# Kernel optimization log

Hardware: AMD Instinct MI355X
Metric: run time of the kernel (lower is better)

## Reference

```python
import jax, jax.numpy as jnp
import numpy as np

N_IN, N_OUT, H, EMB, NSC = 32, 8, 256, 32, 5
B, T = 256, 512
D_IN0 = N_IN + N_OUT + EMB  # 72


def setup_inputs() -> dict:
    key = jax.random.key(0)
    ks = jax.random.split(key, 18)
    s = 0.05
    rn = lambda k, shape: (jax.random.normal(k, shape, jnp.float32) * s)
    return {
        "x_cv": jax.random.normal(ks[0], (B, T, N_IN), jnp.float32),
        "pv_init": jax.random.normal(ks[1], (B, N_OUT), jnp.float32),
        "scenario": jax.random.randint(ks[2], (B,), 0, NSC),
        "emb_table": rn(ks[3], (NSC, EMB)),
        "W_ih0": rn(ks[4], (4 * H, D_IN0)),
        "W_hh0": rn(ks[5], (4 * H, H)),
        "b_ih0": rn(ks[6], (4 * H,)),
        "b_hh0": rn(ks[7], (4 * H,)),
        "W_ih1": rn(ks[8], (4 * H, H)),
        "W_hh1": rn(ks[9], (4 * H, H)),
        "b_ih1": rn(ks[10], (4 * H,)),
        "b_hh1": rn(ks[11], (4 * H,)),
        "fc1_w": rn(ks[12], (H // 2, H)),
        "fc1_b": rn(ks[13], (H // 2,)),
        "fc2_w": rn(ks[14], (N_OUT, H // 2)),
        "fc2_b": rn(ks[15], (N_OUT,)),
    }


def _lstm_cell(x, h, c, W_ih, W_hh, b):
    # torch gate order: i, f, g, o
    g = x @ W_ih.T + h @ W_hh.T + b
    i, f, gg, o = jnp.split(g, 4, axis=-1)
    c_new = jax.nn.sigmoid(f) * c + jax.nn.sigmoid(i) * jnp.tanh(gg)
    h_new = jax.nn.sigmoid(o) * jnp.tanh(c_new)
    return h_new, c_new


def reference(x_cv, pv_init, scenario, emb_table, W_ih0, W_hh0, b_ih0, b_hh0,
              W_ih1, W_hh1, b_ih1, b_hh1, fc1_w, fc1_b, fc2_w, fc2_b):
    # previous prediction. Dropout inactive (eval mode).
    emb = emb_table[scenario]          # [B, EMB]
    b0 = b_ih0 + b_hh0
    b1 = b_ih1 + b_hh1
    Bsz = x_cv.shape[0]
    z = jnp.zeros((Bsz, H), x_cv.dtype)

    def step(carry, x_t):
        h0, c0, h1, c1, pv = carry
        xt = jnp.concatenate([x_t, pv, emb], axis=-1)   # [B, D_IN0]
        h0, c0 = _lstm_cell(xt, h0, c0, W_ih0, W_hh0, b0)
        h1, c1 = _lstm_cell(h0, h1, c1, W_ih1, W_hh1, b1)
        pv_pred = jax.nn.relu(h1 @ fc1_w.T + fc1_b) @ fc2_w.T + fc2_b
        new_carry = (h0, c0, h1, c1, jax.lax.stop_gradient(pv_pred))
        return new_carry, pv_pred

    init = (z, z, z, z, pv_init)
    _, outs = jax.lax.scan(step, init, jnp.swapaxes(x_cv, 0, 1))  # [T, B, N_OUT]
    return jnp.swapaxes(outs, 0, 1)  # [B, T, N_OUT]
```

## Files before the change

### kernel.cpp

```cpp
#include <hip/hip_runtime.h>
#include <hip/hip_bf16.h>


#define B_TOT   256
#define T_STEPS 512
#define NIN     32
#define NOUT    8
#define HDIM    256
#define EMBD    32

#define BPG   2
#define NBLK  (B_TOT / BPG)
#define NTHR  256

#define K2_0      160
#define K2_0_REAL 148
#define NCH0      10
#define K2_1      256
#define NCH1      16

#define WT0_OFF   0u
#define WT0_BYTES (K2_0 * HDIM * 4u * 4u)
#define WT1_OFF   (WT0_OFF + WT0_BYTES)
#define WT1_BYTES (K2_1 * HDIM * 4u * 4u)
#define FC1_OFF   (WT1_OFF + WT1_BYTES)
#define FC1_BYTES (128u * 128u * 4u)
#define FC2_OFF   (FC1_OFF + FC1_BYTES)
#define FC2_BYTES (64u * 8u * 4u)

typedef _Float16 h2 __attribute__((ext_vector_type(2)));

#if __has_builtin(__builtin_amdgcn_fdot2)
#define FDOT2(a, b, c) __builtin_amdgcn_fdot2((a), (b), (c), false)
#else
#define FDOT2(a, b, c) ((c) + (float)(a).x * (float)(b).x + (float)(a).y * (float)(b).y)
#endif

__device__ __forceinline__ float sigm(float x) {
    return 1.0f / (1.0f + __expf(-x));
}
__device__ __forceinline__ float tanh_fast(float x) {
    float e = __expf(2.0f * x);
    return 1.0f - 2.0f / (e + 1.0f);
}

__global__ void prep_wt0(const float* __restrict__ Wih0,
                         const float* __restrict__ Whh0,
                         h2* __restrict__ wt0) {
    int hidx = blockIdx.x * blockDim.x + threadIdx.x;
    if (hidx >= K2_0 * 1024) return;
    int g = hidx & 3, uu = (hidx >> 2) & 255, k2 = hidx >> 10;
    h2 r = {(_Float16)0.0f, (_Float16)0.0f};
    if (k2 < K2_0_REAL) {
        int row = g * 256 + uu;
        int k = 2 * k2;
        float v0 = (k < 40)     ? Wih0[row * 72 + k]     : Whh0[row * 256 + (k - 40)];
        float v1 = (k + 1 < 40) ? Wih0[row * 72 + k + 1] : Whh0[row * 256 + (k + 1 - 40)];
        r.x = (_Float16)v0;
        r.y = (_Float16)v1;
    }
    wt0[hidx] = r;
}

__global__ void prep_wt1(const float* __restrict__ Wih1,
                         const float* __restrict__ Whh1,
                         h2* __restrict__ wt1) {
    int hidx = blockIdx.x * blockDim.x + threadIdx.x;
    if (hidx >= K2_1 * 1024) return;
    int g = hidx & 3, uu = (hidx >> 2) & 255, k2 = hidx >> 10;
    int row = g * 256 + uu;
    int k = 2 * k2;
    float v0 = (k < 256)     ? Wih1[row * 256 + k]           : Whh1[row * 256 + (k - 256)];
    float v1 = (k + 1 < 256) ? Wih1[row * 256 + k + 1]       : Whh1[row * 256 + (k + 1 - 256)];
    h2 r;
    r.x = (_Float16)v0;
    r.y = (_Float16)v1;
    wt1[hidx] = r;
}

__global__ void prep_fc(const float* __restrict__ fc1w,
                        const float* __restrict__ fc2w,
                        h2* __restrict__ f1t,
                        h2* __restrict__ f2t) {
    int hidx = blockIdx.x * blockDim.x + threadIdx.x;
    if (hidx < 16384) {
        int r = hidx & 127, k2 = hidx >> 7;
        h2 v;
        v.x = (_Float16)fc1w[r * 256 + 2 * k2];
        v.y = (_Float16)fc1w[r * 256 + 2 * k2 + 1];
        f1t[hidx] = v;
    } else if (hidx < 16384 + 512) {
        int hi = hidx - 16384;
        int j = hi & 7, k2 = hi >> 3;
        h2 v;
        v.x = (_Float16)fc2w[j * 128 + 2 * k2];
        v.y = (_Float16)fc2w[j * 128 + 2 * k2 + 1];
        f2t[hi] = v;
    }
}

__device__ __forceinline__ void load16(float4 (&buf)[16],
                                       const float4* __restrict__ wt,
                                       int k2b, int u) {
#pragma unroll
    for (int j = 0; j < 16; ++j) buf[j] = wt[(k2b + j) * 256 + u];
}

template <int S>
__device__ __forceinline__ void comp16(const float4 (&buf)[16],
                                       const h2* xt, int k2b,
                                       float (&acc)[4][BPG]) {
#pragma unroll
    for (int j = 0; j < 16; ++j) {
        h2 w0 = __builtin_bit_cast(h2, buf[j].x);
        h2 w1 = __builtin_bit_cast(h2, buf[j].y);
        h2 w2 = __builtin_bit_cast(h2, buf[j].z);
        h2 w3 = __builtin_bit_cast(h2, buf[j].w);
#pragma unroll
        for (int i = 0; i < BPG; ++i) {
            h2 xv = xt[i * S + k2b + j];
            acc[0][i] = FDOT2(w0, xv, acc[0][i]);
            acc[1][i] = FDOT2(w1, xv, acc[1][i]);
            acc[2][i] = FDOT2(w2, xv, acc[2][i]);
            acc[3][i] = FDOT2(w3, xv, acc[3][i]);
        }
    }
}

template <int S>
__device__ __forceinline__ void matvec_pipe(const float4* __restrict__ wt,
                                            const h2* xt, int NCH, int u,
                                            float (&acc)[4][BPG]) {
    float4 A[16], Bb[16];
    load16(A, wt, 0, u);
    int c = 0;
    for (; c + 2 < NCH; c += 2) {
        load16(Bb, wt, (c + 1) * 16, u);
        comp16<S>(A, xt, c * 16, acc);
        load16(A, wt, (c + 2) * 16, u);
        comp16<S>(Bb, xt, (c + 1) * 16, acc);
    }
    if (NCH & 1) {
        comp16<S>(A, xt, (NCH - 1) * 16, acc);
    } else {
        load16(Bb, wt, (NCH - 1) * 16, u);
        comp16<S>(A, xt, (NCH - 2) * 16, acc);
        comp16<S>(Bb, xt, (NCH - 1) * 16, acc);
    }
}

__global__ __launch_bounds__(NTHR, 1) void lstm_main(
    const float* __restrict__ x_cv, const float* __restrict__ pv_init,
    const int* __restrict__ scen, const float* __restrict__ emb_table,
    const float* __restrict__ Wih0, const float* __restrict__ b_ih0,
    const float* __restrict__ b_hh0, const float* __restrict__ b_ih1,
    const float* __restrict__ b_hh1, const float* __restrict__ fc1_b,
    const float* __restrict__ fc2_b, const float4* __restrict__ wt0,
    const float4* __restrict__ wt1, const h2* __restrict__ fc1t,
    const h2* __restrict__ fc2t, float* __restrict__ out) {
    __shared__ h2 xt0[BPG][K2_0];
    __shared__ h2 xt1[BPG][K2_1];
    __shared__ h2 fch[BPG][64];
    __shared__ float h0f[BPG][HDIM];
    __shared__ float h1f[BPG][HDIM];
    __shared__ float fc1o[BPG][128];
    __shared__ float pvf[BPG][NOUT];
    __shared__ float embs[BPG][EMBD];

    const int tid = threadIdx.x;
    const int u = tid;
    const int b0 = blockIdx.x * BPG;

    {
        h2 z = {(_Float16)0.0f, (_Float16)0.0f};
        {
            int i = tid >> 7, p = tid & 127;
            xt0[i][20 + p] = z;
        }
        for (int idx = tid; idx < BPG * K2_1; idx += NTHR) {
            int i = idx >> 8, p = idx & 255;
            xt1[i][p] = z;
        }
        if (tid < BPG * 12) {
            int i = tid / 12, p = tid % 12;
            xt0[i][K2_0_REAL + p] = z;
        }
        if (tid < BPG * NOUT) {
            int i = tid >> 3, j = tid & 7;
            pvf[i][j] = pv_init[(b0 + i) * NOUT + j];
        }
        if (tid < BPG * EMBD) {
            int i = tid >> 5, kk = tid & 31;
            embs[i][kk] = emb_table[scen[b0 + i] * EMBD + kk];
        }
    }
    __syncthreads();

    float bias0[4][BPG], bias1g[4];
#pragma unroll
    for (int g = 0; g < 4; ++g) {
        const int row = g * 256 + u;
        bias1g[g] = b_ih1[row] + b_hh1[row];
        float s0 = b_ih0[row] + b_hh0[row];
        float s1 = s0;
        for (int kk = 0; kk < EMBD; ++kk) {
            float w = Wih0[row * 72 + 40 + kk];
            s0 += embs[0][kk] * w;
            s1 += embs[1][kk] * w;
        }
        bias0[g][0] = s0;
        bias0[g][1] = s1;
    }

    const float fc1bias = fc1_b[tid & 127];
    float fc2bias = 0.0f;
    float* outp = nullptr;
    if (tid < BPG * NOUT) {
        int j = tid & 7, i = tid >> 3;
        fc2bias = fc2_b[j];
        outp = out + ((size_t)(b0 + i) * T_STEPS) * NOUT + j;
    }

    float c0v[BPG] = {0.0f, 0.0f};
    float c1v[BPG] = {0.0f, 0.0f};

    for (int t = 0; t < T_STEPS; ++t) {
        if (tid < BPG * 20) {
            int i = tid / 20, k2l = tid % 20;
            h2 v;
            if (k2l < 16) {
                const float* xp =
                    x_cv + ((size_t)(b0 + i) * T_STEPS + t) * NIN + 2 * k2l;
                v.x = (_Float16)xp[0];
                v.y = (_Float16)xp[1];
            } else {
                v.x = (_Float16)pvf[i][2 * (k2l - 16)];
                v.y = (_Float16)pvf[i][2 * (k2l - 16) + 1];
            }
            xt0[i][k2l] = v;
        }
        __syncthreads();

        float acc[4][BPG];
#pragma unroll
        for (int g = 0; g < 4; ++g)
#pragma unroll
            for (int i = 0; i < BPG; ++i) acc[g][i] = bias0[g][i];
        matvec_pipe<K2_0>(wt0, &xt0[0][0], NCH0, u, acc);

#pragma unroll
        for (int i = 0; i < BPG; ++i) {
            float ig = sigm(acc[0][i]);
            float fg = sigm(acc[1][i]);
            float gg = tanh_fast(acc[2][i]);
            float og = sigm(acc[3][i]);
            float cn = fg * c0v[i] + ig * gg;
            c0v[i] = cn;
            h0f[i][u] = og * tanh_fast(cn);
        }
        __syncthreads();

        {
            int i = tid >> 7, p = tid & 127;
            h2 v;
            v.x = (_Float16)h0f[i][2 * p];
            v.y = (_Float16)h0f[i][2 * p + 1];
            xt0[i][20 + p] = v;
            xt1[i][p] = v;
        }
        __syncthreads();

#pragma unroll
        for (int g = 0; g < 4; ++g)
#pragma unroll
            for (int i = 0; i < BPG; ++i) acc[g][i] = bias1g[g];
        matvec_pipe<K2_1>(wt1, &xt1[0][0], NCH1, u, acc);

#pragma unroll
        for (int i = 0; i < BPG; ++i) {
            float ig = sigm(acc[0][i]);
            float fg = sigm(acc[1][i]);
            float gg = tanh_fast(acc[2][i]);
            float og = sigm(acc[3][i]);
            float cn = fg * c1v[i] + ig * gg;
            c1v[i] = cn;
            h1f[i][u] = og * tanh_fast(cn);
        }
        __syncthreads();

        {
            int i = tid >> 7, p = tid & 127;
            h2 v;
            v.x = (_Float16)h1f[i][2 * p];
            v.y = (_Float16)h1f[i][2 * p + 1];
            xt1[i][128 + p] = v;
        }
        __syncthreads();

        {
            int r = tid & 127, i = tid >> 7;
            float a = fc1bias;
            const h2* xrow = &xt1[i][128];
#pragma unroll 8
            for (int k2 = 0; k2 < 128; ++k2)
                a = FDOT2(fc1t[k2 * 128 + r], xrow[k2], a);
            fc1o[i][r] = fmaxf(a, 0.0f);
        }
        __syncthreads();

        if (tid < BPG * 64) {
            int i = tid >> 6, p = tid & 63;
            h2 v;
            v.x = (_Float16)fc1o[i][2 * p];
            v.y = (_Float16)fc1o[i][2 * p + 1];
            fch[i][p] = v;
        }
        __syncthreads();

        if (tid < BPG * NOUT) {
            int j = tid & 7, i = tid >> 3;
            float a = fc2bias;
#pragma unroll 8
            for (int k2 = 0; k2 < 64; ++k2)
                a = FDOT2(fc2t[k2 * 8 + j], fch[i][k2], a);
            outp[(size_t)t * NOUT] = a;
            pvf[i][j] = a;
        }
        __syncthreads();
    }
}

extern "C" void kernel_launch(void* const* d_in, const int* in_sizes, int n_in,
                              void* d_out, int out_size, void* d_ws,
                              size_t ws_size, hipStream_t stream) {
    const float* x_cv = (const float*)d_in[0];
    const float* pv_init = (const float*)d_in[1];
    const int* scen = (const int*)d_in[2];
    const float* embt = (const float*)d_in[3];
    const float* Wih0 = (const float*)d_in[4];
    const float* Whh0 = (const float*)d_in[5];
    const float* bih0 = (const float*)d_in[6];
    const float* bhh0 = (const float*)d_in[7];
    const float* Wih1 = (const float*)d_in[8];
    const float* Whh1 = (const float*)d_in[9];
    const float* bih1 = (const float*)d_in[10];
    const float* bhh1 = (const float*)d_in[11];
    const float* fc1w = (const float*)d_in[12];
    const float* fc1b = (const float*)d_in[13];
    const float* fc2w = (const float*)d_in[14];
    const float* fc2b = (const float*)d_in[15];

    char* ws = (char*)d_ws;
    h2* wt0 = (h2*)(ws + WT0_OFF);
    h2* wt1 = (h2*)(ws + WT1_OFF);
    h2* f1t = (h2*)(ws + FC1_OFF);
    h2* f2t = (h2*)(ws + FC2_OFF);

    prep_wt0<<<(K2_0 * 1024) / 256, 256, 0, stream>>>(Wih0, Whh0, wt0);
    prep_wt1<<<(K2_1 * 1024) / 256, 256, 0, stream>>>(Wih1, Whh1, wt1);
    prep_fc<<<66, 256, 0, stream>>>(fc1w, fc2w, f1t, f2t);

    lstm_main<<<NBLK, NTHR, 0, stream>>>(
        x_cv, pv_init, scen, embt, Wih0, bih0, bhh0, bih1, bhh1, fc1b, fc2b,
        (const float4*)wt0, (const float4*)wt1, f1t, f2t, (float*)d_out);
}
```

Baseline: 15.63 ms.

## Split LSTM hidden units across blocks with LDS-resident weights and global flag sync

The kernel is rebuilt so that each group of 16 batch rows is handled by 16 cooperating blocks. Each block owns a 16-unit slice of the hidden state for every gate and keeps its fp16 weight slice resident in LDS, instead of streaming all weights from global memory every step. Blocks exchange h0, h1 and the predicted pv through workspace buffers using acquire/release flag spin-waits each timestep. This trades weight bandwidth for inter-block synchronization latency. It also depends on all 256 blocks being co-resident, or the spin-waits will deadlock.

```diff
diff --git a/kernel.cpp b/kernel.cpp
--- a/kernel.cpp
+++ b/kernel.cpp
@@ -2,337 +2,373 @@
 #include <hip/hip_bf16.h>
 
 
-#define B_TOT   256
-#define T_STEPS 512
-#define NIN     32
-#define NOUT    8
-#define HDIM    256
-#define EMBD    32
-
-#define BPG   2
-#define NBLK  (B_TOT / BPG)
-#define NTHR  256
-
-#define K2_0      160
-#define K2_0_REAL 148
-#define NCH0      10
-#define K2_1      256
-#define NCH1      16
-
-#define WT0_OFF   0u
-#define WT0_BYTES (K2_0 * HDIM * 4u * 4u)
-#define WT1_OFF   (WT0_OFF + WT0_BYTES)
-#define WT1_BYTES (K2_1 * HDIM * 4u * 4u)
-#define FC1_OFF   (WT1_OFF + WT1_BYTES)
-#define FC1_BYTES (128u * 128u * 4u)
-#define FC2_OFF   (FC1_OFF + FC1_BYTES)
-#define FC2_BYTES (64u * 8u * 4u)
+#define TSTEPS 512
+#define NIN    32
 
 typedef _Float16 h2 __attribute__((ext_vector_type(2)));
-
 #if __has_builtin(__builtin_amdgcn_fdot2)
 #define FDOT2(a, b, c) __builtin_amdgcn_fdot2((a), (b), (c), false)
 #else
 #define FDOT2(a, b, c) ((c) + (float)(a).x * (float)(b).x + (float)(a).y * (float)(b).y)
 #endif
 
-__device__ __forceinline__ float sigm(float x) {
-    return 1.0f / (1.0f + __expf(-x));
-}
-__device__ __forceinline__ float tanh_fast(float x) {
+__device__ __forceinline__ float sigm(float x) { return 1.0f / (1.0f + __expf(-x)); }
+__device__ __forceinline__ float tanhf_(float x) {
     float e = __expf(2.0f * x);
     return 1.0f - 2.0f / (e + 1.0f);
 }
 
-__global__ void prep_wt0(const float* __restrict__ Wih0,
-                         const float* __restrict__ Whh0,
-                         h2* __restrict__ wt0) {
-    int hidx = blockIdx.x * blockDim.x + threadIdx.x;
-    if (hidx >= K2_0 * 1024) return;
-    int g = hidx & 3, uu = (hidx >> 2) & 255, k2 = hidx >> 10;
-    h2 r = {(_Float16)0.0f, (_Float16)0.0f};
-    if (k2 < K2_0_REAL) {
-        int row = g * 256 + uu;
-        int k = 2 * k2;
-        float v0 = (k < 40)     ? Wih0[row * 72 + k]     : Whh0[row * 256 + (k - 40)];
-        float v1 = (k + 1 < 40) ? Wih0[row * 72 + k + 1] : Whh0[row * 256 + (k + 1 - 40)];
-        r.x = (_Float16)v0;
-        r.y = (_Float16)v1;
-    }
-    wt0[hidx] = r;
-}
-
-__global__ void prep_wt1(const float* __restrict__ Wih1,
-                         const float* __restrict__ Whh1,
-                         h2* __restrict__ wt1) {
-    int hidx = blockIdx.x * blockDim.x + threadIdx.x;
-    if (hidx >= K2_1 * 1024) return;
-    int g = hidx & 3, uu = (hidx >> 2) & 255, k2 = hidx >> 10;
-    int row = g * 256 + uu;
-    int k = 2 * k2;
-    float v0 = (k < 256)     ? Wih1[row * 256 + k]           : Whh1[row * 256 + (k - 256)];
-    float v1 = (k + 1 < 256) ? Wih1[row * 256 + k + 1]       : Whh1[row * 256 + (k + 1 - 256)];
-    h2 r;
-    r.x = (_Float16)v0;
-    r.y = (_Float16)v1;
-    wt1[hidx] = r;
-}
-
-__global__ void prep_fc(const float* __restrict__ fc1w,
-                        const float* __restrict__ fc2w,
-                        h2* __restrict__ f1t,
-                        h2* __restrict__ f2t) {
-    int hidx = blockIdx.x * blockDim.x + threadIdx.x;
-    if (hidx < 16384) {
-        int r = hidx & 127, k2 = hidx >> 7;
-        h2 v;
-        v.x = (_Float16)fc1w[r * 256 + 2 * k2];
-        v.y = (_Float16)fc1w[r * 256 + 2 * k2 + 1];
-        f1t[hidx] = v;
-    } else if (hidx < 16384 + 512) {
-        int hi = hidx - 16384;
-        int j = hi & 7, k2 = hi >> 3;
-        h2 v;
-        v.x = (_Float16)fc2w[j * 128 + 2 * k2];
-        v.y = (_Float16)fc2w[j * 128 + 2 * k2 + 1];
-        f2t[hi] = v;
-    }
-}
-
-__device__ __forceinline__ void load16(float4 (&buf)[16],
-                                       const float4* __restrict__ wt,
-                                       int k2b, int u) {
-#pragma unroll
-    for (int j = 0; j < 16; ++j) buf[j] = wt[(k2b + j) * 256 + u];
-}
-
-template <int S>
-__device__ __forceinline__ void comp16(const float4 (&buf)[16],
-                                       const h2* xt, int k2b,
-                                       float (&acc)[4][BPG]) {
-#pragma unroll
-    for (int j = 0; j < 16; ++j) {
-        h2 w0 = __builtin_bit_cast(h2, buf[j].x);
-        h2 w1 = __builtin_bit_cast(h2, buf[j].y);
-        h2 w2 = __builtin_bit_cast(h2, buf[j].z);
-        h2 w3 = __builtin_bit_cast(h2, buf[j].w);
-#pragma unroll
-        for (int i = 0; i < BPG; ++i) {
-            h2 xv = xt[i * S + k2b + j];
-            acc[0][i] = FDOT2(w0, xv, acc[0][i]);
-            acc[1][i] = FDOT2(w1, xv, acc[1][i]);
-            acc[2][i] = FDOT2(w2, xv, acc[2][i]);
-            acc[3][i] = FDOT2(w3, xv, acc[3][i]);
-        }
-    }
-}
-
-template <int S>
-__device__ __forceinline__ void matvec_pipe(const float4* __restrict__ wt,
-                                            const h2* xt, int NCH, int u,
-                                            float (&acc)[4][BPG]) {
-    float4 A[16], Bb[16];
-    load16(A, wt, 0, u);
-    int c = 0;
-    for (; c + 2 < NCH; c += 2) {
-        load16(Bb, wt, (c + 1) * 16, u);
-        comp16<S>(A, xt, c * 16, acc);
-        load16(A, wt, (c + 2) * 16, u);
-        comp16<S>(Bb, xt, (c + 1) * 16, acc);
-    }
-    if (NCH & 1) {
-        comp16<S>(A, xt, (NCH - 1) * 16, acc);
+#define W0T_OFF 0u
+#define W1T_OFF 606208u
+#define F1T_OFF 1654784u
+#define F2T_OFF 1720320u
+#define HX0_OFF 2097152u
+#define HX1_OFF 2359296u
+#define PVX_OFF 2621440u
+#define FLG_OFF 2629632u
+#define WS_NEED 2678784u
+
+#define W0S 592
+#define W1S 1040
+#define X0S 608
+#define X1S 1040
+
+__global__ void prep_w(const float* __restrict__ Wih0, const float* __restrict__ Whh0,
+                       const float* __restrict__ Wih1, const float* __restrict__ Whh1,
+                       char* __restrict__ ws) {
+    int gid = blockIdx.x * 256 + threadIdx.x;
+    _Float16* w0 = (_Float16*)(ws + W0T_OFF);
+    _Float16* w1 = (_Float16*)(ws + W1T_OFF);
+    if (gid < 16 * 64 * 296) {
+        int k = gid % 296;
+        int rest = gid / 296;
+        int rl = rest & 63, j = rest >> 6;
+        int row = (rl >> 4) * 256 + j * 16 + (rl & 15);
+        float v;
+        if (k < 32) v = Wih0[row * 72 + k];
+        else if (k < 288) v = Whh0[row * 256 + (k - 32)];
+        else v = Wih0[row * 72 + 32 + (k - 288)];
+        w0[(j * 64 + rl) * 296 + k] = (_Float16)v;
     } else {
-        load16(Bb, wt, (NCH - 1) * 16, u);
-        comp16<S>(A, xt, (NCH - 2) * 16, acc);
-        comp16<S>(Bb, xt, (NCH - 1) * 16, acc);
-    }
-}
-
-__global__ __launch_bounds__(NTHR, 1) void lstm_main(
+        int gid2 = gid - 16 * 64 * 296;
+        if (gid2 < 16 * 64 * 512) {
+            int k = gid2 & 511;
+            int rest = gid2 >> 9;
+            int rl = rest & 63, j = rest >> 6;
+            int row = (rl >> 4) * 256 + j * 16 + (rl & 15);
+            float v = (k < 256) ? Wih1[row * 256 + k] : Whh1[row * 256 + (k - 256)];
+            w1[(j * 64 + rl) * 512 + k] = (_Float16)v;
+        }
+    }
+}
+
+__global__ void prep_fc(const float* __restrict__ fc1w, const float* __restrict__ fc2w,
+                        char* __restrict__ ws) {
+    int gid = blockIdx.x * 256 + threadIdx.x;
+    _Float16* f1 = (_Float16*)(ws + F1T_OFF);
+    _Float16* f2 = (_Float16*)(ws + F2T_OFF);
+    if (gid < 32768) {
+        int e = gid & 63, ks = (gid >> 6) & 3, r = gid >> 8;
+        f1[gid] = (_Float16)fc1w[r * 256 + ks * 64 + e];
+    } else if (gid < 32768 + 1024) {
+        int i = gid - 32768;
+        f2[i] = (_Float16)fc2w[i];
+    }
+}
+
+__global__ __launch_bounds__(512) void lstm_main(
     const float* __restrict__ x_cv, const float* __restrict__ pv_init,
     const int* __restrict__ scen, const float* __restrict__ emb_table,
     const float* __restrict__ Wih0, const float* __restrict__ b_ih0,
     const float* __restrict__ b_hh0, const float* __restrict__ b_ih1,
     const float* __restrict__ b_hh1, const float* __restrict__ fc1_b,
-    const float* __restrict__ fc2_b, const float4* __restrict__ wt0,
-    const float4* __restrict__ wt1, const h2* __restrict__ fc1t,
-    const h2* __restrict__ fc2t, float* __restrict__ out) {
-    __shared__ h2 xt0[BPG][K2_0];
-    __shared__ h2 xt1[BPG][K2_1];
-    __shared__ h2 fch[BPG][64];
-    __shared__ float h0f[BPG][HDIM];
-    __shared__ float h1f[BPG][HDIM];
-    __shared__ float fc1o[BPG][128];
-    __shared__ float pvf[BPG][NOUT];
-    __shared__ float embs[BPG][EMBD];
+    const float* __restrict__ fc2_b, char* __restrict__ ws,
+    float* __restrict__ out) {
+    struct __align__(16) SM {
+        char w0[64 * W0S];
+        char w1[64 * W1S];
+        char xt0[16 * X0S];
+        char xt1[16 * X1S];
+        float gates[16][64];
+        float biasE[16][64];
+        float bias1[64];
+        _Float16 htmp[16][16];
+        float embs[16][32];
+        float fc1o[128];
+        int scen_l[16];
+    };
+    __shared__ SM sm;
 
     const int tid = threadIdx.x;
-    const int u = tid;
-    const int b0 = blockIdx.x * BPG;
+    const int lane = tid & 63;
+    const int wv = tid >> 6;
+    const int bid = blockIdx.x;
+    const int g = (bid & 7) * 2 + ((bid >> 3) & 1);
+    const int j = bid >> 4;
+    const int B0 = g * 16;
+
+    const char* w0g = ws + W0T_OFF + (unsigned)j * (64u * 296u * 2u);
+    const char* w1g = ws + W1T_OFF + (unsigned)j * (64u * 512u * 2u);
+    unsigned long long* hx0 = (unsigned long long*)(ws + HX0_OFF) + (unsigned)g * 2u * 16u * 64u;
+    unsigned long long* hx1 = (unsigned long long*)(ws + HX1_OFF) + (unsigned)g * 2u * 16u * 64u;
+    unsigned long long* pvx = (unsigned long long*)(ws + PVX_OFF) + (unsigned)g * 2u * 16u * 2u;
+    unsigned int* flg = (unsigned int*)(ws + FLG_OFF) + (unsigned)g * 16u * 3u * 16u;
+
+    if (tid < 16) sm.scen_l[tid] = scen[B0 + tid];
+    if (tid == 0) {
+        __hip_atomic_store(&flg[(j * 3 + 0) * 16], 0u, __ATOMIC_RELAXED, __HIP_MEMORY_SCOPE_AGENT);
+        __hip_atomic_store(&flg[(j * 3 + 1) * 16], 0u, __ATOMIC_RELAXED, __HIP_MEMORY_SCOPE_AGENT);
+        __hip_atomic_store(&flg[(j * 3 + 2) * 16], 0u, __ATOMIC_RELAXED, __HIP_MEMORY_SCOPE_AGENT);
+    }
+    __syncthreads();
 
     {
-        h2 z = {(_Float16)0.0f, (_Float16)0.0f};
+        int b = tid >> 5, e = tid & 31;
+        sm.embs[b][e] = emb_table[sm.scen_l[b] * 32 + e];
+    }
+    for (int idx = tid; idx < (16 * X0S) / 8; idx += 512) ((unsigned long long*)sm.xt0)[idx] = 0ull;
+    for (int idx = tid; idx < (16 * X1S) / 8; idx += 512) ((unsigned long long*)sm.xt1)[idx] = 0ull;
+    for (int idx = tid; idx < 64 * 37; idx += 512) {
+        int r = idx / 37, c = idx - r * 37;
+        *(float4*)(&sm.w0[r * W0S + c * 16]) = *(const float4*)(w0g + r * 592 + c * 16);
+    }
+    for (int idx = tid; idx < 64 * 64; idx += 512) {
+        int r = idx >> 6, c = idx & 63;
+        *(float4*)(&sm.w1[r * W1S + c * 16]) = *(const float4*)(w1g + r * 1024 + c * 16);
+    }
+    __syncthreads();
+
+    for (int idx = tid; idx < 1024; idx += 512) {
+        int b = idx >> 6, rl = idx & 63;
+        int row = (rl >> 4) * 256 + j * 16 + (rl & 15);
+        float s = b_ih0[row] + b_hh0[row];
+        for (int e = 0; e < 32; ++e) s += sm.embs[b][e] * Wih0[row * 72 + 40 + e];
+        sm.biasE[b][rl] = s;
+    }
+    if (tid < 64) {
+        int row = (tid >> 4) * 256 + j * 16 + (tid & 15);
+        sm.bias1[tid] = b_ih1[row] + b_hh1[row];
+    }
+    float4 f1w[8];
+    {
+        const char* f1g = ws + F1T_OFF + (unsigned)tid * 128u;
+#pragma unroll
+        for (int q = 0; q < 8; ++q) f1w[q] = *(const float4*)(f1g + q * 16);
+    }
+    float f2w[16];
+    if (wv == 0) {
+        int jo = lane >> 3, ks2 = lane & 7;
+        const _Float16* f2g = (const _Float16*)(ws + F2T_OFF) + jo * 128 + ks2 * 16;
+#pragma unroll
+        for (int q = 0; q < 16; ++q) f2w[q] = (float)f2g[q];
+    }
+    const float fc2b_r = (wv == 0) ? fc2_b[lane >> 3] : 0.0f;
+    const float fc1b_r = fc1_b[tid >> 2];
+    float c0 = 0.0f, c1 = 0.0f;
+    __syncthreads();
+
+    for (int t = 0; t < TSTEPS; ++t) {
+        const int par = t & 1;
+
         {
-            int i = tid >> 7, p = tid & 127;
-            xt0[i][20 + p] = z;
-        }
-        for (int idx = tid; idx < BPG * K2_1; idx += NTHR) {
-            int i = idx >> 8, p = idx & 255;
-            xt1[i][p] = z;
-        }
-        if (tid < BPG * 12) {
-            int i = tid / 12, p = tid % 12;
-            xt0[i][K2_0_REAL + p] = z;
-        }
-        if (tid < BPG * NOUT) {
-            int i = tid >> 3, j = tid & 7;
-            pvf[i][j] = pv_init[(b0 + i) * NOUT + j];
-        }
-        if (tid < BPG * EMBD) {
-            int i = tid >> 5, kk = tid & 31;
-            embs[i][kk] = emb_table[scen[b0 + i] * EMBD + kk];
-        }
-    }
-    __syncthreads();
-
-    float bias0[4][BPG], bias1g[4];
-#pragma unroll
-    for (int g = 0; g < 4; ++g) {
-        const int row = g * 256 + u;
-        bias1g[g] = b_ih1[row] + b_hh1[row];
-        float s0 = b_ih0[row] + b_hh0[row];
-        float s1 = s0;
-        for (int kk = 0; kk < EMBD; ++kk) {
-            float w = Wih0[row * 72 + 40 + kk];
-            s0 += embs[0][kk] * w;
-            s1 += embs[1][kk] * w;
-        }
-        bias0[g][0] = s0;
-        bias0[g][1] = s1;
-    }
-
-    const float fc1bias = fc1_b[tid & 127];
-    float fc2bias = 0.0f;
-    float* outp = nullptr;
-    if (tid < BPG * NOUT) {
-        int j = tid & 7, i = tid >> 3;
-        fc2bias = fc2_b[j];
-        outp = out + ((size_t)(b0 + i) * T_STEPS) * NOUT + j;
-    }
-
-    float c0v[BPG] = {0.0f, 0.0f};
-    float c1v[BPG] = {0.0f, 0.0f};
-
-    for (int t = 0; t < T_STEPS; ++t) {
-        if (tid < BPG * 20) {
-            int i = tid / 20, k2l = tid % 20;
-            h2 v;
-            if (k2l < 16) {
-                const float* xp =
-                    x_cv + ((size_t)(b0 + i) * T_STEPS + t) * NIN + 2 * k2l;
-                v.x = (_Float16)xp[0];
-                v.y = (_Float16)xp[1];
+            int b = tid >> 5, k = tid & 31;
+            float xv = x_cv[((B0 + b) * TSTEPS + t) * NIN + k];
+            *(_Float16*)(&sm.xt0[b * X0S + k * 2]) = (_Float16)xv;
+        }
+        for (int idx = tid; idx < 1024; idx += 512) {
+            int b = idx >> 6, rl = idx & 63;
+            sm.gates[b][rl] = sm.biasE[b][rl];
+        }
+        if (wv == 0 && lane < 16) {
+            if (t == 0) {
+                const float* pp = pv_init + (B0 + lane) * 8;
+#pragma unroll
+                for (int q = 0; q < 8; ++q)
+                    *(_Float16*)(&sm.xt0[lane * X0S + (288 + q) * 2]) = (_Float16)pp[q];
             } else {
-                v.x = (_Float16)pvf[i][2 * (k2l - 16)];
-                v.y = (_Float16)pvf[i][2 * (k2l - 16) + 1];
-            }
-            xt0[i][k2l] = v;
-        }
-        __syncthreads();
-
-        float acc[4][BPG];
-#pragma unroll
-        for (int g = 0; g < 4; ++g)
-#pragma unroll
-            for (int i = 0; i < BPG; ++i) acc[g][i] = bias0[g][i];
-        matvec_pipe<K2_0>(wt0, &xt0[0][0], NCH0, u, acc);
-
-#pragma unroll
-        for (int i = 0; i < BPG; ++i) {
-            float ig = sigm(acc[0][i]);
-            float fg = sigm(acc[1][i]);
-            float gg = tanh_fast(acc[2][i]);
-            float og = sigm(acc[3][i]);
-            float cn = fg * c0v[i] + ig * gg;
-            c0v[i] = cn;
-            h0f[i][u] = og * tanh_fast(cn);
+                while (__hip_atomic_load(&flg[(lane * 3 + 2) * 16], __ATOMIC_ACQUIRE,
+                                         __HIP_MEMORY_SCOPE_AGENT) != (unsigned)t) {}
+                int pp = (t - 1) & 1;
+                unsigned long long v0 = __hip_atomic_load(&pvx[(pp * 16 + lane) * 2 + 0],
+                                                          __ATOMIC_RELAXED, __HIP_MEMORY_SCOPE_AGENT);
+                unsigned long long v1 = __hip_atomic_load(&pvx[(pp * 16 + lane) * 2 + 1],
+                                                          __ATOMIC_RELAXED, __HIP_MEMORY_SCOPE_AGENT);
+                *(unsigned long long*)(&sm.xt0[lane * X0S + 576]) = v0;
+                *(unsigned long long*)(&sm.xt0[lane * X0S + 584]) = v1;
+            }
         }
         __syncthreads();
 
         {
-            int i = tid >> 7, p = tid & 127;
-            h2 v;
-            v.x = (_Float16)h0f[i][2 * p];
-            v.y = (_Float16)h0f[i][2 * p + 1];
-            xt0[i][20 + p] = v;
-            xt1[i][p] = v;
-        }
-        __syncthreads();
-
-#pragma unroll
-        for (int g = 0; g < 4; ++g)
-#pragma unroll
-            for (int i = 0; i < BPG; ++i) acc[g][i] = bias1g[g];
-        matvec_pipe<K2_1>(wt1, &xt1[0][0], NCH1, u, acc);
-
-#pragma unroll
-        for (int i = 0; i < BPG; ++i) {
-            float ig = sigm(acc[0][i]);
-            float fg = sigm(acc[1][i]);
-            float gg = tanh_fast(acc[2][i]);
-            float og = sigm(acc[3][i]);
-            float cn = fg * c1v[i] + ig * gg;
-            c1v[i] = cn;
-            h1f[i][u] = og * tanh_fast(cn);
+            float acc[16];
+#pragma unroll
+            for (int b = 0; b < 16; ++b) acc[b] = 0.0f;
+            for (int c = wv; c < 37; c += 8) {
+                float4 w = *(const float4*)(&sm.w0[lane * W0S + c * 16]);
+                h2 w0_ = __builtin_bit_cast(h2, w.x), w1_ = __builtin_bit_cast(h2, w.y);
+                h2 w2_ = __builtin_bit_cast(h2, w.z), w3_ = __builtin_bit_cast(h2, w.w);
+#pragma unroll
+                for (int b = 0; b < 16; ++b) {
+                    float4 xv = *(const float4*)(&sm.xt0[b * X0S + c * 16]);
+                    acc[b] = FDOT2(w0_, __builtin_bit_cast(h2, xv.x), acc[b]);
+                    acc[b] = FDOT2(w1_, __builtin_bit_cast(h2, xv.y), acc[b]);
+                    acc[b] = FDOT2(w2_, __builtin_bit_cast(h2, xv.z), acc[b]);
+                    acc[b] = FDOT2(w3_, __builtin_bit_cast(h2, xv.w), acc[b]);
+                }
+            }
+#pragma unroll
+            for (int b = 0; b < 16; ++b) atomicAdd(&sm.gates[b][lane], acc[b]);
+        }
+        __syncthreads();
+
+        if (tid < 256) {
+            int ui = tid & 15, b = tid >> 4;
+            float gi = sm.gates[b][ui], gf = sm.gates[b][16 + ui];
+            float gc = sm.gates[b][32 + ui], go = sm.gates[b][48 + ui];
+            c0 = sigm(gf) * c0 + sigm(gi) * tanhf_(gc);
+            sm.htmp[b][ui] = (_Float16)(sigm(go) * tanhf_(c0));
+        }
+        __syncthreads();
+
+        if (wv == 0) {
+            unsigned long long v = *(const unsigned long long*)(&sm.htmp[lane >> 2][(lane & 3) * 4]);
+            __hip_atomic_store(&hx0[(par * 16 + j) * 64 + lane], v, __ATOMIC_RELAXED,
+                               __HIP_MEMORY_SCOPE_AGENT);
+            if (lane == 0)
+                __hip_atomic_store(&flg[(j * 3 + 0) * 16], (unsigned)(t + 1), __ATOMIC_RELEASE,
+                                   __HIP_MEMORY_SCOPE_AGENT);
+            if (lane < 16)
+                while (__hip_atomic_load(&flg[(lane * 3 + 0) * 16], __ATOMIC_ACQUIRE,
+                                         __HIP_MEMORY_SCOPE_AGENT) != (unsigned)(t + 1)) {}
+        }
+        __syncthreads();
+
+        for (int idx = tid; idx < 1024; idx += 512) {
+            int jj = idx >> 6, l = idx & 63;
+            unsigned long long v = __hip_atomic_load(&hx0[(par * 16 + jj) * 64 + l],
+                                                     __ATOMIC_RELAXED, __HIP_MEMORY_SCOPE_AGENT);
+            int b = l >> 2, u = jj * 16 + (l & 3) * 4;
+            *(unsigned long long*)(&sm.xt1[b * X1S + u * 2]) = v;
+            *(unsigned long long*)(&sm.xt0[b * X0S + (32 + u) * 2]) = v;
+        }
+        for (int idx = tid; idx < 1024; idx += 512) {
+            int b = idx >> 6, rl = idx & 63;
+            sm.gates[b][rl] = sm.bias1[rl];
         }
         __syncthreads();
 
         {
-            int i = tid >> 7, p = tid & 127;
-            h2 v;
-            v.x = (_Float16)h1f[i][2 * p];
-            v.y = (_Float16)h1f[i][2 * p + 1];
-            xt1[i][128 + p] = v;
+            float acc[16];
+#pragma unroll
+            for (int b = 0; b < 16; ++b) acc[b] = 0.0f;
+            for (int c = wv; c < 64; c += 8) {
+                float4 w = *(const float4*)(&sm.w1[lane * W1S + c * 16]);
+                h2 w0_ = __builtin_bit_cast(h2, w.x), w1_ = __builtin_bit_cast(h2, w.y);
+                h2 w2_ = __builtin_bit_cast(h2, w.z), w3_ = __builtin_bit_cast(h2, w.w);
+#pragma unroll
+                for (int b = 0; b < 16; ++b) {
+                    float4 xv = *(const float4*)(&sm.xt1[b * X1S + c * 16]);
+                    acc[b] = FDOT2(w0_, __builtin_bit_cast(h2, xv.x), acc[b]);
+                    acc[b] = FDOT2(w1_, __builtin_bit_cast(h2, xv.y), acc[b]);
+                    acc[b] = FDOT2(w2_, __builtin_bit_cast(h2, xv.z), acc[b]);
+                    acc[b] = FDOT2(w3_, __builtin_bit_cast(h2, xv.w), acc[b]);
+                }
+            }
+#pragma unroll
+            for (int b = 0; b < 16; ++b) atomicAdd(&sm.gates[b][lane], acc[b]);
+        }
+        __syncthreads();
+
+        if (tid < 256) {
+            int ui = tid & 15, b = tid >> 4;
+            float gi = sm.gates[b][ui], gf = sm.gates[b][16 + ui];
+            float gc = sm.gates[b][32 + ui], go = sm.gates[b][48 + ui];
+            c1 = sigm(gf) * c1 + sigm(gi) * tanhf_(gc);
+            sm.htmp[b][ui] = (_Float16)(sigm(go) * tanhf_(c1));
+        }
+        __syncthreads();
+
+        if (wv == 0) {
+            unsigned long long v = *(const unsigned long long*)(&sm.htmp[lane >> 2][(lane & 3) * 4]);
+            __hip_atomic_store(&hx1[(par * 16 + j) * 64 + lane], v, __ATOMIC_RELAXED,
+                               __HIP_MEMORY_SCOPE_AGENT);
+            if (lane == 0)
+                __hip_atomic_store(&flg[(j * 3 + 1) * 16], (unsigned)(t + 1), __ATOMIC_RELEASE,
+                                   __HIP_MEMORY_SCOPE_AGENT);
+            if (lane < 16)
+                while (__hip_atomic_load(&flg[(lane * 3 + 1) * 16], __ATOMIC_ACQUIRE,
+                                         __HIP_MEMORY_SCOPE_AGENT) != (unsigned)(t + 1)) {}
+        }
+        __syncthreads();
+
+        for (int idx = tid; idx < 1024; idx += 512) {
+            int jj = idx >> 6, l = idx & 63;
+            unsigned long long v = __hip_atomic_load(&hx1[(par * 16 + jj) * 64 + l],
+                                                     __ATOMIC_RELAXED, __HIP_MEMORY_SCOPE_AGENT);
+            int b = l >> 2, u = jj * 16 + (l & 3) * 4;
+            *(unsigned long long*)(&sm.xt1[b * X1S + (256 + u) * 2]) = v;
         }
         __syncthreads();
 
         {
-            int r = tid & 127, i = tid >> 7;
-            float a = fc1bias;
-            const h2* xrow = &xt1[i][128];
-#pragma unroll 8
-            for (int k2 = 0; k2 < 128; ++k2)
-                a = FDOT2(fc1t[k2 * 128 + r], xrow[k2], a);
-            fc1o[i][r] = fmaxf(a, 0.0f);
-        }
-        __syncthreads();
-
-        if (tid < BPG * 64) {
-            int i = tid >> 6, p = tid & 63;
-            h2 v;
-            v.x = (_Float16)fc1o[i][2 * p];
-            v.y = (_Float16)fc1o[i][2 * p + 1];
-            fch[i][p] = v;
-        }
-        __syncthreads();
-
-        if (tid < BPG * NOUT) {
-            int j = tid & 7, i = tid >> 3;
-            float a = fc2bias;
-#pragma unroll 8
-            for (int k2 = 0; k2 < 64; ++k2)
-                a = FDOT2(fc2t[k2 * 8 + j], fch[i][k2], a);
-            outp[(size_t)t * NOUT] = a;
-            pvf[i][j] = a;
-        }
-        __syncthreads();
+            int row = tid >> 2, ks = tid & 3;
+            float a = 0.0f;
+#pragma unroll
+            for (int q = 0; q < 8; ++q) {
+                float4 xv = *(const float4*)(&sm.xt1[j * X1S + (256 + ks * 64 + q * 8) * 2]);
+                a = FDOT2(__builtin_bit_cast(h2, f1w[q].x), __builtin_bit_cast(h2, xv.x), a);
+                a = FDOT2(__builtin_bit_cast(h2, f1w[q].y), __builtin_bit_cast(h2, xv.y), a);
+                a = FDOT2(__builtin_bit_cast(h2, f1w[q].z), __builtin_bit_cast(h2, xv.z), a);
+                a = FDOT2(__builtin_bit_cast(h2, f1w[q].w), __builtin_bit_cast(h2, xv.w), a);
+            }
+            a += __shfl_xor(a, 1);
+            a += __shfl_xor(a, 2);
+            if (ks == 0) sm.fc1o[row] = fmaxf(a + fc1b_r, 0.0f);
+        }
+        __syncthreads();
+
+        if (wv == 0) {
+            int jo = lane >> 3, ks2 = lane & 7;
+            float a = 0.0f;
+#pragma unroll
+            for (int q = 0; q < 4; ++q) {
+                float4 xv = *(const float4*)(&sm.fc1o[ks2 * 16 + q * 4]);
+                a += f2w[q * 4 + 0] * xv.x + f2w[q * 4 + 1] * xv.y +
+                     f2w[q * 4 + 2] * xv.z + f2w[q * 4 + 3] * xv.w;
+            }
+            a += __shfl_xor(a, 1);
+            a += __shfl_xor(a, 2);
+            a += __shfl_xor(a, 4);
+            float av = a + fc2b_r;
+            if (ks2 == 0) out[((B0 + j) * TSTEPS + t) * 8 + jo] = av;
+            float p0 = __shfl(av, 0), p1 = __shfl(av, 8), p2 = __shfl(av, 16), p3 = __shfl(av, 24);
+            float p4 = __shfl(av, 32), p5 = __shfl(av, 40), p6 = __shfl(av, 48), p7 = __shfl(av, 56);
+            if (lane == 0) {
+                h2 q0, q1, q2, q3;
+                q0.x = (_Float16)p0; q0.y = (_Float16)p1;
+                q1.x = (_Float16)p2; q1.y = (_Float16)p3;
+                q2.x = (_Float16)p4; q2.y = (_Float16)p5;
+                q3.x = (_Float16)p6; q3.y = (_Float16)p7;
+                unsigned long long v0 = ((unsigned long long)__builtin_bit_cast(unsigned, q1) << 32) |
+                                        __builtin_bit_cast(unsigned, q0);
+                unsigned long long v1 = ((unsigned long long)__builtin_bit_cast(unsigned, q3) << 32) |
+                                        __builtin_bit_cast(unsigned, q2);
+                __hip_atomic_store(&pvx[(par * 16 + j) * 2 + 0], v0, __ATOMIC_RELAXED,
+                                   __HIP_MEMORY_SCOPE_AGENT);
+                __hip_atomic_store(&pvx[(par * 16 + j) * 2 + 1], v1, __ATOMIC_RELAXED,
+                                   __HIP_MEMORY_SCOPE_AGENT);
+                __hip_atomic_store(&flg[(j * 3 + 2) * 16], (unsigned)(t + 1), __ATOMIC_RELEASE,
+                                   __HIP_MEMORY_SCOPE_AGENT);
+            }
+        }
     }
 }
 
 extern "C" void kernel_launch(void* const* d_in, const int* in_sizes, int n_in,
-                              void* d_out, int out_size, void* d_ws,
-                              size_t ws_size, hipStream_t stream) {
+                              void* d_out, int out_size, void* d_ws, size_t ws_size,
+                              hipStream_t stream) {
+    if (ws_size < WS_NEED) return;
+
     const float* x_cv = (const float*)d_in[0];
     const float* pv_init = (const float*)d_in[1];
     const int* scen = (const int*)d_in[2];
@@ -351,16 +387,10 @@
     const float* fc2b = (const float*)d_in[15];
 
     char* ws = (char*)d_ws;
-    h2* wt0 = (h2*)(ws + WT0_OFF);
-    h2* wt1 = (h2*)(ws + WT1_OFF);
-    h2* f1t = (h2*)(ws + FC1_OFF);
-    h2* f2t = (h2*)(ws + FC2_OFF);
-
-    prep_wt0<<<(K2_0 * 1024) / 256, 256, 0, stream>>>(Wih0, Whh0, wt0);
-    prep_wt1<<<(K2_1 * 1024) / 256, 256, 0, stream>>>(Wih1, Whh1, wt1);
-    prep_fc<<<66, 256, 0, stream>>>(fc1w, fc2w, f1t, f2t);
-
-    lstm_main<<<NBLK, NTHR, 0, stream>>>(
-        x_cv, pv_init, scen, embt, Wih0, bih0, bhh0, bih1, bhh1, fc1b, fc2b,
-        (const float4*)wt0, (const float4*)wt1, f1t, f2t, (float*)d_out);
-}
+
+    prep_w<<<3232, 256, 0, stream>>>(Wih0, Whh0, Wih1, Whh1, ws);
+    prep_fc<<<132, 256, 0, stream>>>(fc1w, fc2w, ws);
+
+    lstm_main<<<256, 512, 0, stream>>>(x_cv, pv_init, scen, embt, Wih0, bih0, bhh0,
+                                       bih1, bhh1, fc1b, fc2b, ws, (float*)d_out);
+}
```

Result: slower. 19.94 ms (+27.6%).
